# Kernel tuning notes

Hardware: AMD Instinct MI355X
Metric: run time of the kernel (lower is better)

Reference implementation:

```python
import jax, jax.numpy as jnp
import numpy as np

BASE = 10000.0

def positional_encoding(seq_len, dim, dtype=jnp.float32):
    # standard sinusoidal PE: pe[p, 2i] = sin(p / BASE^(2i/dim)), pe[p, 2i+1] = cos(...)
    pos = jnp.arange(seq_len, dtype=dtype)[:, None]            # [S,1]
    idx = jnp.arange(0, dim, 2, dtype=dtype)[None, :]          # [1,dim/2]
    ang = pos / jnp.power(BASE, idx / dim)                     # [S,dim/2]
    pe = jnp.zeros((seq_len, dim), dtype=dtype)
    pe = pe.at[:, 0::2].set(jnp.sin(ang)).at[:, 1::2].set(jnp.cos(ang))
    return pe

def setup_inputs() -> dict:
    key = jax.random.key(0)
    ks = jax.random.split(key, 5)
    B, S, H, D = 16, 2048, 128, 64
    x = jax.random.normal(ks[0], (B, S, H), dtype=jnp.float32)
    Wq = jax.random.normal(ks[1], (H, D), dtype=jnp.float32) * (H ** -0.5)
    Wk = jax.random.normal(ks[2], (H, D), dtype=jnp.float32) * (H ** -0.5)
    Wv = jax.random.normal(ks[3], (H, D), dtype=jnp.float32) * (H ** -0.5)
    Wf = jax.random.normal(ks[4], (D, 1), dtype=jnp.float32) * (D ** -0.5)
    bf = jnp.zeros((1,), dtype=jnp.float32)
    return {"x": x, "Wq": Wq, "Wk": Wk, "Wv": Wv, "Wf": Wf, "bf": bf}

def reference(x, Wq, Wk, Wv, Wf, bf):
    B, S, H = x.shape
    xp = x + positional_encoding(S, H, x.dtype)[None]          # add PE, broadcast over batch
    Q = jnp.einsum('bsh,hd->bsd', xp, Wq)
    K = jnp.einsum('bsh,hd->bsd', xp, Wk)
    V = jnp.einsum('bsh,hd->bsd', xp, Wv)
    D = K.shape[-1]
    scores = jnp.einsum('bqd,bkd->bqk', Q, K) / jnp.sqrt(jnp.asarray(D, x.dtype))
    # NOTE: softmax over dim=1 (the QUERY axis), per the original nn.Softmax(dim=1)
    attn = jax.nn.softmax(scores, axis=1)                      # [B,S,S]
    z = jnp.einsum('bqk,bkd->bqd', attn, V)                    # [B,S,D]
    out = (jnp.einsum('bsd,do->bso', z, Wf) + bf).squeeze(-1)  # [B,S]
    return out
```

## Files before the change

kernel.cpp:

```cpp
#include <hip/hip_runtime.h>
#include <hip/hip_bf16.h>
#include <math.h>

#define BATCH 16
#define SEQ   2048
#define HID   128
#define DIM   64

typedef __attribute__((ext_vector_type(8))) short bf16x8;
typedef __attribute__((ext_vector_type(4))) float f32x4;

#define QSCALE 0.18033688011112042f
#define C0_PE  0.07195578314043169f

static __device__ __forceinline__ ushort f2bf(float f) {
    union { float f; unsigned u; } v; v.f = f;
    unsigned r = v.u + 0x7FFFu + ((v.u >> 16) & 1u);
    return (ushort)(r >> 16);
}

static __device__ __forceinline__ float fast_exp2(float x) {
#if __has_builtin(__builtin_amdgcn_exp2f)
    return __builtin_amdgcn_exp2f(x);
#else
    return exp2f(x);
#endif
}

__global__ __launch_bounds__(256) void k_prep(
    const float* __restrict__ Wq, const float* __restrict__ Wk,
    const float* __restrict__ Wv, const float* __restrict__ Wf,
    ushort* __restrict__ Wt, float* __restrict__ wvf) {
    const int gid = blockIdx.x * 256 + threadIdx.x;
    if (gid < HID) {
        float s = 0.f;
        #pragma unroll 8
        for (int d = 0; d < DIM; ++d) s += Wv[gid * DIM + d] * Wf[d];
        wvf[gid] = s;
    }
    if (gid < 128 * 128) {
        int col = gid >> 7, k = gid & 127;
        float v = (col < 64) ? Wq[k * DIM + col] * QSCALE : Wk[k * DIM + (col - 64)];
        Wt[gid] = f2bf(v);
    }
}

__global__ __launch_bounds__(256) void k_qkv(
    const float* __restrict__ x, const ushort* __restrict__ Wt,
    const float* __restrict__ wvf, ushort* __restrict__ Qb,
    ushort* __restrict__ Kb, float* __restrict__ vf)
{
    const int tid  = threadIdx.x;
    const int wave = tid >> 6;
    const int lane = tid & 63;
    const int quad = lane >> 4;
    const int col  = lane & 15;
    const int rowbase = blockIdx.x * 64 + wave * 16;
    const int grow = rowbase + col;
    const float pos = (float)(grow & (SEQ - 1));

    bf16x8 af[4];
    float vpart = 0.f;
    #pragma unroll
    for (int c = 0; c < 4; ++c) {
        const float* xp = x + (size_t)grow * HID + quad * 8 + c * 32;
        float4 v0 = *(const float4*)(xp);
        float4 v1 = *(const float4*)(xp + 4);
        float t[8] = {v0.x, v0.y, v0.z, v0.w, v1.x, v1.y, v1.z, v1.w};
        #pragma unroll
        for (int jp = 0; jp < 4; ++jp) {
            int h = quad * 8 + c * 32 + jp * 2;
            float ang = pos * __expf(-(float)h * C0_PE);
            t[jp * 2]     += __sinf(ang);
            t[jp * 2 + 1] += __cosf(ang);
        }
        const float* wp = wvf + quad * 8 + c * 32;
        float4 w0 = *(const float4*)(wp);
        float4 w1 = *(const float4*)(wp + 4);
        vpart += t[0] * w0.x + t[1] * w0.y + t[2] * w0.z + t[3] * w0.w +
                 t[4] * w1.x + t[5] * w1.y + t[6] * w1.z + t[7] * w1.w;
        short* ap = (short*)&af[c];
        #pragma unroll
        for (int j = 0; j < 8; ++j) ap[j] = (short)f2bf(t[j]);
    }

    vpart += __shfl_xor(vpart, 16);
    vpart += __shfl_xor(vpart, 32);
    if (quad == 0) vf[grow] = vpart;

    #pragma unroll
    for (int t = 0; t < 8; ++t) {
        const ushort* wrow = Wt + (size_t)(t * 16 + col) * 128 + quad * 8;
        f32x4 acc = {0.f, 0.f, 0.f, 0.f};
        #pragma unroll
        for (int c = 0; c < 4; ++c) {
            bf16x8 bfr = *(const bf16x8*)(wrow + c * 32);
            acc = __builtin_amdgcn_mfma_f32_16x16x32_bf16(af[c], bfr, acc, 0, 0, 0);
        }
        const int cb = (t & 3) * 16 + col;
        ushort* dst = (t < 4) ? Qb : Kb;
        const int r0 = rowbase + quad * 4;
        #pragma unroll
        for (int r = 0; r < 4; ++r)
            dst[(size_t)(r0 + r) * DIM + cb] = f2bf(acc[r]);
    }
}

__global__ __launch_bounds__(1024) void k_attn(
    const ushort* __restrict__ Qb, const ushort* __restrict__ Kb,
    const float* __restrict__ vf, const float* __restrict__ bfp,
    float* __restrict__ outp)
{
    const int b    = blockIdx.y;
    const int k0   = blockIdx.x * 64;
    const int tid  = threadIdx.x;
    const int wave = tid >> 6;
    const int lane = tid & 63;
    const int quad = lane >> 4;
    const int col  = lane & 15;

    __shared__ float sl[16][64];
    __shared__ float wcol[64];

    bf16x8 kf[4][2];
    {
        const ushort* Kbase = Kb + ((size_t)(b * SEQ + k0)) * DIM;
        #pragma unroll
        for (int t = 0; t < 4; ++t)
            #pragma unroll
            for (int c = 0; c < 2; ++c)
                kf[t][c] = *(const bf16x8*)(Kbase + (size_t)(t * 16 + col) * DIM + quad * 8 + c * 32);
    }

    const ushort* Qstart = Qb + ((size_t)(b * SEQ + wave * 128 + col)) * DIM + quad * 8;

    float l[4] = {0.f, 0.f, 0.f, 0.f};
    {
        const ushort* Qrow = Qstart;
        for (int qi = 0; qi < 8; ++qi) {
            bf16x8 a0 = *(const bf16x8*)(Qrow);
            bf16x8 a1 = *(const bf16x8*)(Qrow + 32);
            Qrow += 16 * DIM;
            #pragma unroll
            for (int t = 0; t < 4; ++t) {
                f32x4 acc = {0.f, 0.f, 0.f, 0.f};
                acc = __builtin_amdgcn_mfma_f32_16x16x32_bf16(a0, kf[t][0], acc, 0, 0, 0);
                acc = __builtin_amdgcn_mfma_f32_16x16x32_bf16(a1, kf[t][1], acc, 0, 0, 0);
                l[t] += fast_exp2(acc.x) + fast_exp2(acc.y) +
                        fast_exp2(acc.z) + fast_exp2(acc.w);
            }
        }
    }
    #pragma unroll
    for (int t = 0; t < 4; ++t) {
        l[t] += __shfl_xor(l[t], 16);
        l[t] += __shfl_xor(l[t], 32);
    }
    if (quad == 0) {
        #pragma unroll
        for (int t = 0; t < 4; ++t) sl[wave][t * 16 + col] = l[t];
    }
    __syncthreads();
    if (tid < 64) {
        float ll = 0.f;
        #pragma unroll
        for (int w = 0; w < 16; ++w) ll += sl[w][tid];
        wcol[tid] = vf[(size_t)b * SEQ + k0 + tid] / ll;
    }
    __syncthreads();

    const float bias = bfp[0] * (1.0f / (SEQ / 64));
    float wreg[4];
    #pragma unroll
    for (int t = 0; t < 4; ++t) wreg[t] = wcol[t * 16 + col];

    {
        const ushort* Qrow = Qstart;
        float* outb = outp + (size_t)b * SEQ;
        for (int qi = 0; qi < 8; ++qi) {
            bf16x8 a0 = *(const bf16x8*)(Qrow);
            bf16x8 a1 = *(const bf16x8*)(Qrow + 32);
            Qrow += 16 * DIM;
            float rs[4] = {0.f, 0.f, 0.f, 0.f};
            #pragma unroll
            for (int t = 0; t < 4; ++t) {
                f32x4 acc = {0.f, 0.f, 0.f, 0.f};
                acc = __builtin_amdgcn_mfma_f32_16x16x32_bf16(a0, kf[t][0], acc, 0, 0, 0);
                acc = __builtin_amdgcn_mfma_f32_16x16x32_bf16(a1, kf[t][1], acc, 0, 0, 0);
                #pragma unroll
                for (int r = 0; r < 4; ++r)
                    rs[r] += fast_exp2(acc[r]) * wreg[t];
            }
            #pragma unroll
            for (int r = 0; r < 4; ++r) {
                float v = rs[r];
                v += __shfl_xor(v, 1); v += __shfl_xor(v, 2);
                v += __shfl_xor(v, 4); v += __shfl_xor(v, 8);
                rs[r] = v;
            }
            if (col == 0) {
                const int qrow = wave * 128 + qi * 16 + quad * 4;
                #pragma unroll
                for (int r = 0; r < 4; ++r)
                    atomicAdd(&outb[qrow + r], rs[r] + bias);
            }
        }
    }
}

extern "C" void kernel_launch(void* const* d_in, const int* in_sizes, int n_in,
                              void* d_out, int out_size, void* d_ws, size_t ws_size,
                              hipStream_t stream) {
    (void)in_sizes; (void)n_in; (void)ws_size;
    const float* x  = (const float*)d_in[0];
    const float* Wq = (const float*)d_in[1];
    const float* Wk = (const float*)d_in[2];
    const float* Wv = (const float*)d_in[3];
    const float* Wf = (const float*)d_in[4];
    const float* bf = (const float*)d_in[5];
    float* outp = (float*)d_out;

    float*  wvf = (float*)d_ws;
    float*  vf  = wvf + 256;
    ushort* Wt  = (ushort*)(vf + (size_t)BATCH * SEQ);
    ushort* Qb  = Wt + 128 * 128;
    ushort* Kb  = Qb + (size_t)BATCH * SEQ * DIM;

    hipMemsetAsync(d_out, 0, (size_t)out_size * sizeof(float), stream);
    k_prep<<<64, 256, 0, stream>>>(Wq, Wk, Wv, Wf, Wt, wvf);
    k_qkv<<<BATCH * SEQ / 64, 256, 0, stream>>>(x, Wt, wvf, Qb, Kb, vf);
    k_attn<<<dim3(SEQ / 64, BATCH), 1024, 0, stream>>>(Qb, Kb, vf, bf, outp);
}
```

Before: 130.8 us.

## Precompute positional-encoding table once and prefetch Q fragments in attention loops

k_prep now builds an S×H float table of sin/cos positional encodings, and k_qkv loads it instead of evaluating exp, sin and cos per element for every batch. The table is computed inside the timed launch, so no work is skipped, but it adds 1 MB of extra global reads in exchange for removing transcendental math. The attention kernel also software-prefetches the next Q fragment before the MFMAs, to hide load latency at the cost of more registers. The inline-asm exp fallback only applies when the builtin is missing, so it probably never runs.

```diff
diff --git a/kernel.cpp b/kernel.cpp
--- a/kernel.cpp
+++ b/kernel.cpp
@@ -23,14 +23,16 @@
 #if __has_builtin(__builtin_amdgcn_exp2f)
     return __builtin_amdgcn_exp2f(x);
 #else
-    return exp2f(x);
+    float r;
+    asm("v_exp_f32 %0, %1\n\ts_nop 1" : "=v"(r) : "v"(x));
+    return r;
 #endif
 }
 
 __global__ __launch_bounds__(256) void k_prep(
     const float* __restrict__ Wq, const float* __restrict__ Wk,
     const float* __restrict__ Wv, const float* __restrict__ Wf,
-    ushort* __restrict__ Wt, float* __restrict__ wvf) {
+    ushort* __restrict__ Wt, float* __restrict__ wvf, float* __restrict__ pe) {
     const int gid = blockIdx.x * 256 + threadIdx.x;
     if (gid < HID) {
         float s = 0.f;
@@ -43,12 +45,18 @@
         float v = (col < 64) ? Wq[k * DIM + col] * QSCALE : Wk[k * DIM + (col - 64)];
         Wt[gid] = f2bf(v);
     }
+    {
+        int s = gid >> 7, h = gid & 127;
+        int he = h & ~1;
+        float ang = (float)s * __expf(-(float)he * C0_PE);
+        pe[gid] = (h & 1) ? __cosf(ang) : __sinf(ang);
+    }
 }
 
 __global__ __launch_bounds__(256) void k_qkv(
     const float* __restrict__ x, const ushort* __restrict__ Wt,
-    const float* __restrict__ wvf, ushort* __restrict__ Qb,
-    ushort* __restrict__ Kb, float* __restrict__ vf)
+    const float* __restrict__ wvf, const float* __restrict__ pe,
+    ushort* __restrict__ Qb, ushort* __restrict__ Kb, float* __restrict__ vf)
 {
     const int tid  = threadIdx.x;
     const int wave = tid >> 6;
@@ -57,7 +65,7 @@
     const int col  = lane & 15;
     const int rowbase = blockIdx.x * 64 + wave * 16;
     const int grow = rowbase + col;
-    const float pos = (float)(grow & (SEQ - 1));
+    const int srow = grow & (SEQ - 1);
 
     bf16x8 af[4];
     float vpart = 0.f;
@@ -66,14 +74,11 @@
         const float* xp = x + (size_t)grow * HID + quad * 8 + c * 32;
         float4 v0 = *(const float4*)(xp);
         float4 v1 = *(const float4*)(xp + 4);
-        float t[8] = {v0.x, v0.y, v0.z, v0.w, v1.x, v1.y, v1.z, v1.w};
-        #pragma unroll
-        for (int jp = 0; jp < 4; ++jp) {
-            int h = quad * 8 + c * 32 + jp * 2;
-            float ang = pos * __expf(-(float)h * C0_PE);
-            t[jp * 2]     += __sinf(ang);
-            t[jp * 2 + 1] += __cosf(ang);
-        }
+        const float* per = pe + (size_t)srow * HID + quad * 8 + c * 32;
+        float4 p0 = *(const float4*)(per);
+        float4 p1 = *(const float4*)(per + 4);
+        float t[8] = {v0.x + p0.x, v0.y + p0.y, v0.z + p0.z, v0.w + p0.w,
+                      v1.x + p1.x, v1.y + p1.y, v1.z + p1.z, v1.w + p1.w};
         const float* wp = wvf + quad * 8 + c * 32;
         float4 w0 = *(const float4*)(wp);
         float4 w1 = *(const float4*)(wp + 4);
@@ -137,9 +142,14 @@
     float l[4] = {0.f, 0.f, 0.f, 0.f};
     {
         const ushort* Qrow = Qstart;
+        bf16x8 a0 = *(const bf16x8*)(Qrow);
+        bf16x8 a1 = *(const bf16x8*)(Qrow + 32);
         for (int qi = 0; qi < 8; ++qi) {
-            bf16x8 a0 = *(const bf16x8*)(Qrow);
-            bf16x8 a1 = *(const bf16x8*)(Qrow + 32);
+            bf16x8 n0, n1;
+            if (qi < 7) {
+                n0 = *(const bf16x8*)(Qrow + 16 * DIM);
+                n1 = *(const bf16x8*)(Qrow + 16 * DIM + 32);
+            }
             Qrow += 16 * DIM;
             #pragma unroll
             for (int t = 0; t < 4; ++t) {
@@ -149,6 +159,7 @@
                 l[t] += fast_exp2(acc.x) + fast_exp2(acc.y) +
                         fast_exp2(acc.z) + fast_exp2(acc.w);
             }
+            a0 = n0; a1 = n1;
         }
     }
     #pragma unroll
@@ -177,9 +188,14 @@
     {
         const ushort* Qrow = Qstart;
         float* outb = outp + (size_t)b * SEQ;
+        bf16x8 a0 = *(const bf16x8*)(Qrow);
+        bf16x8 a1 = *(const bf16x8*)(Qrow + 32);
         for (int qi = 0; qi < 8; ++qi) {
-            bf16x8 a0 = *(const bf16x8*)(Qrow);
-            bf16x8 a1 = *(const bf16x8*)(Qrow + 32);
+            bf16x8 n0, n1;
+            if (qi < 7) {
+                n0 = *(const bf16x8*)(Qrow + 16 * DIM);
+                n1 = *(const bf16x8*)(Qrow + 16 * DIM + 32);
+            }
             Qrow += 16 * DIM;
             float rs[4] = {0.f, 0.f, 0.f, 0.f};
             #pragma unroll
@@ -191,6 +207,7 @@
                 for (int r = 0; r < 4; ++r)
                     rs[r] += fast_exp2(acc[r]) * wreg[t];
             }
+            a0 = n0; a1 = n1;
             #pragma unroll
             for (int r = 0; r < 4; ++r) {
                 float v = rs[r];
@@ -222,12 +239,13 @@
 
     float*  wvf = (float*)d_ws;
     float*  vf  = wvf + 256;
-    ushort* Wt  = (ushort*)(vf + (size_t)BATCH * SEQ);
+    float*  pe  = vf + (size_t)BATCH * SEQ;
+    ushort* Wt  = (ushort*)(pe + (size_t)SEQ * HID);
     ushort* Qb  = Wt + 128 * 128;
     ushort* Kb  = Qb + (size_t)BATCH * SEQ * DIM;
 
     hipMemsetAsync(d_out, 0, (size_t)out_size * sizeof(float), stream);
-    k_prep<<<64, 256, 0, stream>>>(Wq, Wk, Wv, Wf, Wt, wvf);
-    k_qkv<<<BATCH * SEQ / 64, 256, 0, stream>>>(x, Wt, wvf, Qb, Kb, vf);
+    k_prep<<<SEQ * HID / 256, 256, 0, stream>>>(Wq, Wk, Wv, Wf, Wt, wvf, pe);
+    k_qkv<<<BATCH * SEQ / 64, 256, 0, stream>>>(x, Wt, wvf, pe, Qb, Kb, vf);
     k_attn<<<dim3(SEQ / 64, BATCH), 1024, 0, stream>>>(Qb, Kb, vf, bf, outp);
 }
```

Result: slower. 135.3 us (+3.4%).
